# Performance work log

Measured on AMD Instinct MI355X. Metric: run time of the kernel, lower is better.

The kernel has to match this reference:

```python
import jax, jax.numpy as jnp
import numpy as np

SEQ, BATCH, INPUT = 2048, 64, 16
HEADS, HID = 8, 64  # per-head hidden = hidden_size/output_size = 512/8


def setup_inputs() -> dict:
    key = jax.random.key(0)
    ks = jax.random.split(key, 8)
    s = 1.0 / np.sqrt(HID)  # PyTorch LSTM/Linear init scale
    return {
        "x": jax.random.normal(ks[0], (SEQ, BATCH, INPUT), jnp.float32),
        "W_ih": jax.random.uniform(ks[1], (HEADS, 4 * HID, INPUT), jnp.float32, -s, s),
        "W_hh": jax.random.uniform(ks[2], (HEADS, 4 * HID, HID), jnp.float32, -s, s),
        "b_ih": jax.random.uniform(ks[3], (HEADS, 4 * HID), jnp.float32, -s, s),
        "b_hh": jax.random.uniform(ks[4], (HEADS, 4 * HID), jnp.float32, -s, s),
        "W_lin": jax.random.uniform(ks[5], (HEADS, HID), jnp.float32, -s, s),
        "b_lin": jax.random.uniform(ks[6], (HEADS,), jnp.float32, -s, s),
    }


def _multihead_lstm(x, W_ih, W_hh, b_ih, b_hh):
    # x: (T,B,I); weights stacked over heads H. PyTorch gate order: i,f,g,o.
    T, B = x.shape[0], x.shape[1]
    H, G = W_hh.shape[0], W_hh.shape[1]  # G = 4*hid
    hid = G // 4
    # Input projection for all timesteps/heads at once: (T,B,H,4h)
    xp = jnp.einsum("tbi,hgi->tbhg", x, W_ih) + b_ih + b_hh

    def step(carry, xt):
        h_prev, c_prev = carry  # (B,H,hid)
        z = xt + jnp.einsum("bhk,hgk->bhg", h_prev, W_hh)  # (B,H,4h)
        i = jax.nn.sigmoid(z[..., 0 * hid:1 * hid])
        f = jax.nn.sigmoid(z[..., 1 * hid:2 * hid])
        g = jnp.tanh(z[..., 2 * hid:3 * hid])
        o = jax.nn.sigmoid(z[..., 3 * hid:4 * hid])
        c = f * c_prev + i * g
        h = o * jnp.tanh(c)
        return (h, c), h

    zeros = jnp.zeros((B, H, hid), x.dtype)
    _, hs = jax.lax.scan(step, (zeros, zeros), xp)  # hs: (T,B,H,hid)
    return hs


def reference(x, W_ih, W_hh, b_ih, b_hh, W_lin, b_lin):
    hs = _multihead_lstm(x, W_ih, W_hh, b_ih, b_hh)  # (T,B,H,hid)
    # per-head Linear(hid -> 1), concatenated over heads -> (T,B,H)
    out = jnp.einsum("tbhk,hk->tbh", hs, W_lin) + b_lin
    # lstm_output accumulates (sums) the per-head hidden trajectories
    lstm_output = hs.sum(axis=2)  # (T,B,hid)
    return out, lstm_output
```

## Files before the change

kernel.cpp:

```cpp
#include <hip/hip_runtime.h>
#include <hip/hip_fp16.h>

#define TT   2048
#define BB   64
#define II   16
#define HH   8
#define HIDN 64
#define GG   256
#define T4   (TT / 4)

typedef _Float16 h2 __attribute__((ext_vector_type(2)));
typedef _Float16 h4 __attribute__((ext_vector_type(4)));
typedef _Float16 h8 __attribute__((ext_vector_type(8)));
typedef float    f4 __attribute__((ext_vector_type(4)));

__device__ __forceinline__ float fdot2(h2 a, h2 b, float c) {
    return __builtin_amdgcn_fdot2(a, b, c, false);
}
__device__ __forceinline__ float fast_sigmoid(float z) {
    return __builtin_amdgcn_rcpf(1.0f + __expf(-z));
}
__device__ __forceinline__ float fast_tanh(float z) {
    return fmaf(2.0f, __builtin_amdgcn_rcpf(1.0f + __expf(-2.0f * z)), -1.0f);
}

__device__ __forceinline__ int lds_off(int b, int u) {
    return b * 128 + ((((u >> 3) ^ b) & 7) << 4) + (u & 7) * 2;
}
__device__ __forceinline__ h8 cvt8(const float* p) {
    float4 v0 = ((const float4*)p)[0];
    float4 v1 = ((const float4*)p)[1];
    return h8{(_Float16)v0.x, (_Float16)v0.y, (_Float16)v0.z, (_Float16)v0.w,
              (_Float16)v1.x, (_Float16)v1.y, (_Float16)v1.z, (_Float16)v1.w};
}

__device__ __forceinline__ void sync_lds() {
    asm volatile("s_waitcnt lgkmcnt(0)" ::: "memory");
    __builtin_amdgcn_s_barrier();
    asm volatile("" ::: "memory");
}

__global__ void cvt_x_kernel(const float* __restrict__ x, _Float16* __restrict__ xh, int n4) {
    int i = blockIdx.x * blockDim.x + threadIdx.x;
    if (i < n4) {
        float4 v = ((const float4*)x)[i];
        ((h2*)xh)[2 * i]     = h2{ (_Float16)v.x, (_Float16)v.y };
        ((h2*)xh)[2 * i + 1] = h2{ (_Float16)v.z, (_Float16)v.w };
    }
}

__global__ __launch_bounds__(1024)
void lstm_mfma(const _Float16* __restrict__ xh,
               const float* __restrict__ Wih,
               const float* __restrict__ Whh,
               const float* __restrict__ bih,
               const float* __restrict__ bhh,
               _Float16* __restrict__ stage_f16)
{
    const int tid  = threadIdx.x;
    const int w    = tid >> 6;
    const int lane = tid & 63;
    const int hi   = lane >> 4;
    const int bl   = lane & 15;
    const int hd   = blockIdx.x >> 2;
    const int bg   = blockIdx.x & 3;
    const int ue   = 4 * w + hi;

    const int rA = hd * GG + (bl & 3) * HIDN + 4 * w + (bl >> 2);
    const float* pw = Whh + (size_t)rA * HIDN;
    h8 a0 = cvt8(pw + hi * 8);
    h8 a1 = cvt8(pw + 32 + hi * 8);
    h8 a2{};
    if (hi < 2) a2 = cvt8(Wih + (size_t)rA * II + hi * 8);

    f4 biasv;
#pragma unroll
    for (int g = 0; g < 4; ++g) {
        int r = hd * GG + g * HIDN + ue;
        biasv[g] = bih[r] + bhh[r];
    }

    __shared__ __align__(16) char hA[2048];
    __shared__ __align__(16) char hB[2048];

    const int off_b0 = lds_off(bl, hi * 8);
    const int off_b1 = lds_off(bl, 32 + hi * 8);
    const int off_hw = lds_off(bl, ue);

    const _Float16* xlane = xh + (size_t)(bg * 16 + bl) * II + (hi & 1) * 8;
    auto ldx = [&](int t) -> h8 {
        int tc = t < TT ? t : TT - 1;
        return *(const h8*)(xlane + (size_t)tc * (BB * II));
    };

    *(_Float16*)(hA + off_hw) = (_Float16)0.0f;
    h8 xp0 = ldx(0), xp1 = ldx(1), xp2 = ldx(2), xp3 = ldx(3);
    sync_lds();

    float cst = 0.0f;
    h4* sptr = (h4*)stage_f16 + (size_t)(hd * 64 + bg * 16 + bl) * 64 + ue;

#define STEP(jj, CURH, NXTH, XP) do {                                           \
        f4 acc = __builtin_amdgcn_mfma_f32_16x16x32_f16(a2, XP, biasv, 0,0,0);  \
        XP = ldx(t0 + jj + 4);            \
        h8 vb0 = *(const h8*)(CURH + off_b0);                                   \
        h8 vb1 = *(const h8*)(CURH + off_b1);                                   \
        acc = __builtin_amdgcn_mfma_f32_16x16x32_f16(a0, vb0, acc, 0, 0, 0);    \
        acc = __builtin_amdgcn_mfma_f32_16x16x32_f16(a1, vb1, acc, 0, 0, 0);    \
        float gi = fast_sigmoid(acc[0]);                                        \
        float gf = fast_sigmoid(acc[1]);                                        \
        float gg = fast_tanh(acc[2]);                                           \
        float go = fast_sigmoid(acc[3]);                                        \
        cst = fmaf(gf, cst, gi * gg);                                           \
        float hv = go * fast_tanh(cst);                                         \
        _Float16 h16 = (_Float16)hv;                                            \
        *(_Float16*)(NXTH + off_hw) = h16;                                      \
        hp.p2[jj >> 1][jj & 1] = h16;                                           \
        sync_lds();                                                             \
    } while (0)

    for (int t4 = 0; t4 < T4; ++t4) {
        const int t0 = 4 * t4;
        union { h4 v4; h2 p2[2]; } hp;
        STEP(0, hA, hB, xp0);
        STEP(1, hB, hA, xp1);
        STEP(2, hA, hB, xp2);
        STEP(3, hB, hA, xp3);
        *sptr = hp.v4;
        sptr += 512 * 64;
    }
#undef STEP
}

template <int STAGE, bool XF16>
__global__ __launch_bounds__(64, 1)
void lstm_wave(const float* __restrict__ x,
               const _Float16* __restrict__ xh,
               const float* __restrict__ Wih,
               const float* __restrict__ Whh,
               const float* __restrict__ bih,
               const float* __restrict__ bhh,
               const float* __restrict__ Wlin,
               const float* __restrict__ blin,
               float* __restrict__ out,
               float* __restrict__ lstm_out,
               _Float16* __restrict__ stage_f16)
{
    const int lane = threadIdx.x;
    const int c    = blockIdx.x;
    const int b    = c & (BB - 1);
    const int hd   = c >> 6;

    h2 whh[4][HIDN / 2];
    h2 wih[4][II / 2];
    float bias[4];
#pragma unroll
    for (int g = 0; g < 4; ++g) {
        const int r = hd * GG + g * HIDN + lane;
        const float4* p = (const float4*)(Whh + (size_t)r * HIDN);
#pragma unroll
        for (int q = 0; q < HIDN / 4; ++q) {
            float4 v = p[q];
            whh[g][2 * q]     = h2{ (_Float16)v.x, (_Float16)v.y };
            whh[g][2 * q + 1] = h2{ (_Float16)v.z, (_Float16)v.w };
        }
        const float4* pi = (const float4*)(Wih + (size_t)r * II);
#pragma unroll
        for (int q = 0; q < II / 4; ++q) {
            float4 v = pi[q];
            wih[g][2 * q]     = h2{ (_Float16)v.x, (_Float16)v.y };
            wih[g][2 * q + 1] = h2{ (_Float16)v.z, (_Float16)v.w };
        }
        bias[g] = bih[r] + bhh[r];
    }
    float wl = 0.0f, blv = 0.0f;
    if (STAGE == 2) { wl = Wlin[hd * HIDN + lane]; blv = blin[hd]; }

    __shared__ __align__(16) _Float16 hbuf[HIDN];
    hbuf[lane] = (_Float16)0.0f;

    float cst = 0.0f;

    const _Float16* xhp = xh + b * II;
    const float*    xfp = x + b * II;
    h2 xv[II / 2];
    auto load_x = [&](int t, h2* dst) {
        int tc = t < TT ? t : TT - 1;
        if (XF16) {
            const h8* p = (const h8*)(xhp + (size_t)tc * BB * II);
            union { h8 v; h2 p2[4]; } u0, u1;
            u0.v = p[0];
            u1.v = p[1];
#pragma unroll
            for (int i = 0; i < 4; ++i) { dst[i] = u0.p2[i]; dst[4 + i] = u1.p2[i]; }
        } else {
            const float4* p = (const float4*)(xfp + (size_t)tc * BB * II);
#pragma unroll
            for (int q = 0; q < 4; ++q) {
                float4 v = p[q];
                dst[2 * q]     = h2{ (_Float16)v.x, (_Float16)v.y };
                dst[2 * q + 1] = h2{ (_Float16)v.z, (_Float16)v.w };
            }
        }
    };
    load_x(0, xv);

    h4* sptr = (h4*)(stage_f16 + (size_t)c * 256 + lane * 4);

    for (int t4 = 0; t4 < T4; ++t4) {
        union { h4 v4; h2 p2[2]; } hp;
#pragma unroll
        for (int j = 0; j < 4; ++j) {
            const int t = t4 * 4 + j;
            h2 xn[II / 2];
            load_x(t + 1, xn);

            union { h8 v[8]; h2 p[32]; } hr;
#pragma unroll
            for (int q = 0; q < 8; ++q) hr.v[q] = ((const h8*)hbuf)[q];

            float z0 = bias[0], z1 = bias[1], z2 = bias[2], z3 = bias[3];
#pragma unroll
            for (int q = 0; q < HIDN / 2; ++q) {
                z0 = fdot2(whh[0][q], hr.p[q], z0);
                z1 = fdot2(whh[1][q], hr.p[q], z1);
                z2 = fdot2(whh[2][q], hr.p[q], z2);
                z3 = fdot2(whh[3][q], hr.p[q], z3);
            }
#pragma unroll
            for (int q = 0; q < II / 2; ++q) {
                z0 = fdot2(wih[0][q], xv[q], z0);
                z1 = fdot2(wih[1][q], xv[q], z1);
                z2 = fdot2(wih[2][q], xv[q], z2);
                z3 = fdot2(wih[3][q], xv[q], z3);
            }

            float gi = fast_sigmoid(z0);
            float gf = fast_sigmoid(z1);
            float gg = fast_tanh(z2);
            float go = fast_sigmoid(z3);

            cst = fmaf(gf, cst, gi * gg);
            float h = go * fast_tanh(cst);
            _Float16 h16 = (_Float16)h;

            hbuf[lane] = h16;
            hp.p2[j >> 1][j & 1] = h16;

            if (STAGE == 2) {
                atomicAdd(&lstm_out[((size_t)t * BB + b) * HIDN + lane], h);
                float p = h * wl;
                p += __shfl_down(p, 32, 64);
                p += __shfl_down(p, 16, 64);
                p += __shfl_down(p, 8, 64);
                p += __shfl_down(p, 4, 64);
                p += __shfl_down(p, 2, 64);
                p += __shfl_down(p, 1, 64);
                if (lane == 0) out[((size_t)t * BB + b) * HH + hd] = p + blv;
            }

#pragma unroll
            for (int q = 0; q < II / 2; ++q) xv[q] = xn[q];
        }
        if (STAGE == 1) {
            *sptr = hp.v4;
            sptr += 512 * 64;
        }
    }
}

__global__ __launch_bounds__(256)
void pass_lstm(const _Float16* __restrict__ stage, float* __restrict__ lstm_out)
{
    const int tid  = threadIdx.x;
    const int k    = tid & (HIDN - 1);
    const int q    = tid >> 6;
    const int b    = blockIdx.x & (BB - 1);
    const int tile = blockIdx.x >> 6;
    const h4* sp = (const h4*)stage;

#pragma unroll
    for (int g = 0; g < 4; ++g) {
        const int t4 = tile * 16 + q + 4 * g;
        float acc0 = 0.f, acc1 = 0.f, acc2 = 0.f, acc3 = 0.f;
#pragma unroll
        for (int hd = 0; hd < HH; ++hd) {
            h4 v = sp[((size_t)t4 * 512 + hd * 64 + b) * 64 + k];
            acc0 += (float)v.x; acc1 += (float)v.y;
            acc2 += (float)v.z; acc3 += (float)v.w;
        }
        const size_t t = (size_t)t4 * 4;
        lstm_out[((t + 0) * BB + b) * HIDN + k] = acc0;
        lstm_out[((t + 1) * BB + b) * HIDN + k] = acc1;
        lstm_out[((t + 2) * BB + b) * HIDN + k] = acc2;
        lstm_out[((t + 3) * BB + b) * HIDN + k] = acc3;
    }
}

__global__ __launch_bounds__(512)
void pass_out(const _Float16* __restrict__ stage,
              const float* __restrict__ Wlin,
              const float* __restrict__ blin,
              float* __restrict__ out)
{
    __shared__ float wls[GG * 2];
    const int tid = threadIdx.x;
    wls[tid] = Wlin[tid];
    __syncthreads();

    const int b  = tid >> 3;
    const int hd = tid & 7;
    const int c  = hd * 64 + b;
    const int t4 = blockIdx.x;
    const float bl = blin[hd];

    const h4* sp = (const h4*)stage + ((size_t)t4 * 512 + c) * 64;
    float a0 = 0.f, a1 = 0.f, a2 = 0.f, a3 = 0.f;
#pragma unroll 8
    for (int k = 0; k < HIDN; ++k) {
        h4 v = sp[k];
        float w = wls[hd * HIDN + k];
        a0 = fmaf((float)v.x, w, a0);
        a1 = fmaf((float)v.y, w, a1);
        a2 = fmaf((float)v.z, w, a2);
        a3 = fmaf((float)v.w, w, a3);
    }
    const size_t t = (size_t)t4 * 4;
    out[(t + 0) * 512 + tid] = a0 + bl;
    out[(t + 1) * 512 + tid] = a1 + bl;
    out[(t + 2) * 512 + tid] = a2 + bl;
    out[(t + 3) * 512 + tid] = a3 + bl;
}

extern "C" void kernel_launch(void* const* d_in, const int* in_sizes, int n_in,
                              void* d_out, int out_size, void* d_ws, size_t ws_size,
                              hipStream_t stream)
{
    const float* x    = (const float*)d_in[0];
    const float* Wih  = (const float*)d_in[1];
    const float* Whh  = (const float*)d_in[2];
    const float* bih  = (const float*)d_in[3];
    const float* bhh  = (const float*)d_in[4];
    const float* Wlin = (const float*)d_in[5];
    const float* blin = (const float*)d_in[6];

    float* out  = (float*)d_out;
    float* lstm = out + (size_t)TT * BB * HH;

    const size_t xbytes = (size_t)TT * BB * II * 2 + 4096;
    const size_t slab16 = (size_t)TT * BB * HH * HIDN * 2;

    const bool xf16 = ws_size >= xbytes;
    _Float16* xh = (_Float16*)d_ws;
    char* slabp  = (char*)d_ws + (xf16 ? xbytes : 0);
    size_t avail = ws_size - (xf16 ? xbytes : 0);
    const int mode = (avail >= slab16) ? 1 : 2;

    if (xf16) {
        int n4 = TT * BB * II / 4;
        cvt_x_kernel<<<(n4 + 255) / 256, 256, 0, stream>>>(x, xh, n4);
    }

    _Float16* sh = (_Float16*)slabp;

    if (mode == 1 && xf16) {
        lstm_mfma<<<dim3(HH * 4), dim3(1024), 0, stream>>>(xh, Wih, Whh, bih, bhh, sh);
        pass_lstm<<<dim3(BB * 32), dim3(256), 0, stream>>>(sh, lstm);
        pass_out <<<dim3(T4), dim3(512), 0, stream>>>(sh, Wlin, blin, out);
    } else if (mode == 1) {
        dim3 grid(BB * HH), block(64);
        lstm_wave<1, false><<<grid, block, 0, stream>>>(x, xh, Wih, Whh, bih, bhh,
                                                        Wlin, blin, out, lstm, sh);
        pass_lstm<<<dim3(BB * 32), dim3(256), 0, stream>>>(sh, lstm);
        pass_out <<<dim3(T4), dim3(512), 0, stream>>>(sh, Wlin, blin, out);
    } else {
        hipMemsetAsync(lstm, 0, (size_t)TT * BB * HIDN * 4, stream);
        dim3 grid(BB * HH), block(64);
        if (xf16)
            lstm_wave<2, true><<<grid, block, 0, stream>>>(x, xh, Wih, Whh, bih, bhh,
                                                           Wlin, blin, out, lstm, sh);
        else
            lstm_wave<2, false><<<grid, block, 0, stream>>>(x, xh, Wih, Whh, bih, bhh,
                                                            Wlin, blin, out, lstm, sh);
    }
}
```

Measured before the change: 1.098 ms.

## Coarsen LSTM MFMA block to four waves each computing four M-tiles

The recurrent MFMA kernel drops from 16 waves per block to 4. Each wave now holds four weight tiles and runs four independent MFMA chains and gate computations per timestep, so the per-step LDS barrier has far fewer waves to wait for and each wave gets more instruction-level parallelism. The clamp on the x prefetch index is also removed, which saves a compare per load. In exchange, register pressure per wave rises, the serial work per wave grows, and the unclamped prefetch reads a few rows past the end of the x buffer into the rest of the workspace.

```diff
diff --git a/kernel.cpp b/kernel.cpp
--- a/kernel.cpp
+++ b/kernel.cpp
@@ -49,7 +49,7 @@
     }
 }
 
-__global__ __launch_bounds__(1024)
+__global__ __launch_bounds__(256)
 void lstm_mfma(const _Float16* __restrict__ xh,
                const float* __restrict__ Wih,
                const float* __restrict__ Whh,
@@ -64,20 +64,23 @@
     const int bl   = lane & 15;
     const int hd   = blockIdx.x >> 2;
     const int bg   = blockIdx.x & 3;
-    const int ue   = 4 * w + hi;
-
-    const int rA = hd * GG + (bl & 3) * HIDN + 4 * w + (bl >> 2);
-    const float* pw = Whh + (size_t)rA * HIDN;
-    h8 a0 = cvt8(pw + hi * 8);
-    h8 a1 = cvt8(pw + 32 + hi * 8);
-    h8 a2{};
-    if (hi < 2) a2 = cvt8(Wih + (size_t)rA * II + hi * 8);
-
-    f4 biasv;
-#pragma unroll
-    for (int g = 0; g < 4; ++g) {
-        int r = hd * GG + g * HIDN + ue;
-        biasv[g] = bih[r] + bhh[r];
+
+    h8 a0[4], a1[4], a2[4];
+    f4 biasv[4];
+#pragma unroll
+    for (int mt = 0; mt < 4; ++mt) {
+        const int rA = hd * GG + (bl & 3) * HIDN + 16 * w + 4 * mt + (bl >> 2);
+        const float* pw = Whh + (size_t)rA * HIDN;
+        a0[mt] = cvt8(pw + hi * 8);
+        a1[mt] = cvt8(pw + 32 + hi * 8);
+        a2[mt] = h8{};
+        if (hi < 2) a2[mt] = cvt8(Wih + (size_t)rA * II + hi * 8);
+        const int u = 16 * w + 4 * mt + hi;
+#pragma unroll
+        for (int g = 0; g < 4; ++g) {
+            int r = hd * GG + g * HIDN + u;
+            biasv[mt][g] = bih[r] + bhh[r];
+        }
     }
 
     __shared__ __align__(16) char hA[2048];
@@ -85,49 +88,66 @@
 
     const int off_b0 = lds_off(bl, hi * 8);
     const int off_b1 = lds_off(bl, 32 + hi * 8);
-    const int off_hw = lds_off(bl, ue);
+    int off_hw[4];
+#pragma unroll
+    for (int mt = 0; mt < 4; ++mt) off_hw[mt] = lds_off(bl, 16 * w + 4 * mt + hi);
 
     const _Float16* xlane = xh + (size_t)(bg * 16 + bl) * II + (hi & 1) * 8;
     auto ldx = [&](int t) -> h8 {
-        int tc = t < TT ? t : TT - 1;
-        return *(const h8*)(xlane + (size_t)tc * (BB * II));
+        return *(const h8*)(xlane + (size_t)t * (BB * II));
     };
 
-    *(_Float16*)(hA + off_hw) = (_Float16)0.0f;
+#pragma unroll
+    for (int mt = 0; mt < 4; ++mt) *(_Float16*)(hA + off_hw[mt]) = (_Float16)0.0f;
     h8 xp0 = ldx(0), xp1 = ldx(1), xp2 = ldx(2), xp3 = ldx(3);
     sync_lds();
 
-    float cst = 0.0f;
-    h4* sptr = (h4*)stage_f16 + (size_t)(hd * 64 + bg * 16 + bl) * 64 + ue;
+    float cst[4] = {0.f, 0.f, 0.f, 0.f};
+    h4* sbase = (h4*)stage_f16 + (size_t)(hd * 64 + bg * 16 + bl) * 64 + 16 * w + hi;
 
 #define STEP(jj, CURH, NXTH, XP) do {                                           \
-        f4 acc = __builtin_amdgcn_mfma_f32_16x16x32_f16(a2, XP, biasv, 0,0,0);  \
-        XP = ldx(t0 + jj + 4);            \
+        f4 acc[4];                                                              \
+        _Pragma("unroll")                                                       \
+        for (int mt = 0; mt < 4; ++mt)                                          \
+            acc[mt] = __builtin_amdgcn_mfma_f32_16x16x32_f16(a2[mt], XP,        \
+                                                             biasv[mt], 0,0,0); \
+        XP = ldx(t0 + jj + 4);              \
         h8 vb0 = *(const h8*)(CURH + off_b0);                                   \
         h8 vb1 = *(const h8*)(CURH + off_b1);                                   \
-        acc = __builtin_amdgcn_mfma_f32_16x16x32_f16(a0, vb0, acc, 0, 0, 0);    \
-        acc = __builtin_amdgcn_mfma_f32_16x16x32_f16(a1, vb1, acc, 0, 0, 0);    \
-        float gi = fast_sigmoid(acc[0]);                                        \
-        float gf = fast_sigmoid(acc[1]);                                        \
-        float gg = fast_tanh(acc[2]);                                           \
-        float go = fast_sigmoid(acc[3]);                                        \
-        cst = fmaf(gf, cst, gi * gg);                                           \
-        float hv = go * fast_tanh(cst);                                         \
-        _Float16 h16 = (_Float16)hv;                                            \
-        *(_Float16*)(NXTH + off_hw) = h16;                                      \
-        hp.p2[jj >> 1][jj & 1] = h16;                                           \
+        _Pragma("unroll")                                                       \
+        for (int mt = 0; mt < 4; ++mt)                                          \
+            acc[mt] = __builtin_amdgcn_mfma_f32_16x16x32_f16(a0[mt], vb0,       \
+                                                             acc[mt], 0, 0, 0); \
+        _Pragma("unroll")                                                       \
+        for (int mt = 0; mt < 4; ++mt)                                          \
+            acc[mt] = __builtin_amdgcn_mfma_f32_16x16x32_f16(a1[mt], vb1,       \
+                                                             acc[mt], 0, 0, 0); \
+        _Pragma("unroll")                                                       \
+        for (int mt = 0; mt < 4; ++mt) {                                        \
+            float gi = fast_sigmoid(acc[mt][0]);                                \
+            float gf = fast_sigmoid(acc[mt][1]);                                \
+            float gg = fast_tanh(acc[mt][2]);                                   \
+            float go = fast_sigmoid(acc[mt][3]);                                \
+            cst[mt] = fmaf(gf, cst[mt], gi * gg);                               \
+            float hv = go * fast_tanh(cst[mt]);                                 \
+            _Float16 h16 = (_Float16)hv;                                        \
+            *(_Float16*)(NXTH + off_hw[mt]) = h16;                              \
+            hpk[mt].e[jj] = h16;                                                \
+        }                                                                       \
         sync_lds();                                                             \
     } while (0)
 
     for (int t4 = 0; t4 < T4; ++t4) {
         const int t0 = 4 * t4;
-        union { h4 v4; h2 p2[2]; } hp;
+        union { h4 v4; _Float16 e[4]; } hpk[4];
         STEP(0, hA, hB, xp0);
         STEP(1, hB, hA, xp1);
         STEP(2, hA, hB, xp2);
         STEP(3, hB, hA, xp3);
-        *sptr = hp.v4;
-        sptr += 512 * 64;
+#pragma unroll
+        for (int mt = 0; mt < 4; ++mt)
+            sbase[4 * mt] = hpk[mt].v4;
+        sbase += 512 * 64;
     }
 #undef STEP
 }
@@ -364,7 +384,7 @@
     _Float16* sh = (_Float16*)slabp;
 
     if (mode == 1 && xf16) {
-        lstm_mfma<<<dim3(HH * 4), dim3(1024), 0, stream>>>(xh, Wih, Whh, bih, bhh, sh);
+        lstm_mfma<<<dim3(HH * 4), dim3(256), 0, stream>>>(xh, Wih, Whh, bih, bhh, sh);
         pass_lstm<<<dim3(BB * 32), dim3(256), 0, stream>>>(sh, lstm);
         pass_out <<<dim3(T4), dim3(512), 0, stream>>>(sh, Wlin, blin, out);
     } else if (mode == 1) {
```

Measured after the change: 1.289 ms. 17.4% more time.
